# Optimization experiments

Measured on AMD Instinct MI355X. Metric: run time of the kernel, lower is better.

Reference implementation:

```python
import jax, jax.numpy as jnp
import numpy as np

SEQ_LEN = 2048
DIM = 1024
K = 24
N_FFT = 4096  # nearest power of two >= 2*seq_len - 1


def setup_inputs() -> dict:
    key = jax.random.key(0)
    k1, k2, k3, k4 = jax.random.split(key, 4)
    x = jax.random.normal(k1, (4, SEQ_LEN, DIM), dtype=jnp.float32)
    filters = jax.random.normal(k2, (SEQ_LEN, K), dtype=jnp.float32) * 0.1
    M_inputs = jax.random.normal(k3, (DIM, DIM), dtype=jnp.float32) * (DIM ** -0.5)
    M_filters = jax.random.normal(k4, (K, DIM), dtype=jnp.float32) * (K ** -0.5)
    input_pos = jnp.arange(SEQ_LEN, dtype=jnp.int32)
    return {"x": x, "filters": filters, "M_inputs": M_inputs,
            "M_filters": M_filters, "input_pos": input_pos}


def reference(x, filters, M_inputs, M_filters, input_pos):
    # STU forward, use_approx=True, use_hankel_L=False, no flash_fft, no cache.
    B, S, D = x.shape
    # alternating sign +1,-1,+1,... along sequence
    sgn = jnp.where(jnp.arange(S) % 2 == 0, 1.0, -1.0).astype(x.dtype)[None, :, None]
    x_proj = x @ M_inputs                      # (B, S, D)
    phi_proj = filters @ M_filters             # (S, D)
    # v: (1, S, D, 1) -> rfft over seq axis with length N_FFT
    V = jnp.fft.rfft(phi_proj[None, :, :, None], n=N_FFT, axis=1)
    # U: stack [u, u*sgn] on last axis -> (B, S, D, 2)
    U = jnp.fft.rfft(jnp.stack([x_proj, x_proj * sgn], axis=-1), n=N_FFT, axis=1)
    U_conv = jnp.fft.irfft(V * U, n=N_FFT, axis=1)[:, :S]   # (B, S, D, 2)
    spectral_plus = U_conv[..., 0]
    spectral_minus = U_conv[..., 1] * sgn
    return spectral_plus + spectral_minus
```

## Files before the change

kernel.cpp:

```cpp
#include <hip/hip_runtime.h>
#include <hip/hip_bf16.h>
#include <stdint.h>
#include <stddef.h>

#define DIM 1024
#define SEQ 2048
#define KF 24

using f32x4    = __attribute__((ext_vector_type(4))) float;
using bf16x8   = __attribute__((ext_vector_type(8))) short;
using uint32x4 = __attribute__((ext_vector_type(4))) unsigned int;

__device__ __forceinline__ unsigned short f2bf(float f){
  union { float f; unsigned int i; } v; v.f = f;
  unsigned int r = v.i + 0x7FFFu + ((v.i >> 16) & 1u);
  return (unsigned short)(r >> 16);
}
__device__ __forceinline__ float dot2bf(unsigned int a, unsigned int b, float c){
  float d;
  asm("v_dot2_f32_bf16 %0, %1, %2, %3" : "=v"(d) : "v"(a), "v"(b), "v"(c));
  return d;
}
__device__ __forceinline__ unsigned vext(const uint32x4 v, int i){
  return i == 0 ? v.x : i == 1 ? v.y : i == 2 ? v.z : v.w;
}
__device__ __forceinline__ void gload_lds16(const void* g, void* l){
  __builtin_amdgcn_global_load_lds(
      (const __attribute__((address_space(1))) unsigned int*)g,
      (__attribute__((address_space(3))) unsigned int*)l, 16, 0, 0);
}
__device__ __forceinline__ uint32x4 make_srsrc(const void* base, unsigned bytes){
  uint32x4 r;
  r.x = (unsigned)(uintptr_t)base;
  r.y = (unsigned)((uintptr_t)base >> 32);
  r.z = bytes;
  r.w = 0x00020000u;
  return r;
}

__global__ void k_cvt_x(const float* __restrict__ x, unsigned short* __restrict__ xb){
  int i = blockIdx.x * 256 + threadIdx.x;
  const float4* x4 = (const float4*)x;
  float4 v = x4[i];
  ushort4 o;
  o.x = f2bf(v.x); o.y = f2bf(v.y); o.z = f2bf(v.z); o.w = f2bf(v.w);
  *(ushort4*)(xb + (size_t)i * 4) = o;
}

__global__ void k_tr_M(const float* __restrict__ Mi, unsigned short* __restrict__ MbT){
  __shared__ float tile[32][33];
  int e0 = blockIdx.y * 32, d0 = blockIdx.x * 32;
  int tx = threadIdx.x, ty = threadIdx.y;
  #pragma unroll
  for (int r = 0; r < 32; r += 8)
    tile[ty + r][tx] = Mi[(size_t)(e0 + ty + r) * DIM + d0 + tx];
  __syncthreads();
  #pragma unroll
  for (int r = 0; r < 32; r += 8)
    MbT[(size_t)(d0 + ty + r) * DIM + e0 + tx] = f2bf(tile[tx][ty + r]);
}

__global__ void k_pe(const float* __restrict__ filters, const float* __restrict__ Mf,
                     unsigned int* __restrict__ pepkT){
  int r2 = blockIdx.x * 256 + threadIdx.x;
  int d  = blockIdx.y;
  float a0 = 0.f, a1 = 0.f;
  #pragma unroll
  for (int k = 0; k < KF; ++k){
    float mf = Mf[(size_t)k * DIM + d];
    a0 += filters[(size_t)(4 * r2)     * KF + k] * mf;
    a1 += filters[(size_t)(4 * r2 + 2) * KF + k] * mf;
  }
  unsigned int lo = f2bf(2.f * a0), hi = f2bf(2.f * a1);
  pepkT[(size_t)d * 512 + r2] = lo | (hi << 16);
}

#define BM 128
#define BN 128
#define BKK 64
__global__ void k_gemm(const unsigned short* __restrict__ A,
                       const unsigned short* __restrict__ Bt,
                       unsigned int* __restrict__ Bg){
  __shared__ unsigned short As[BM * BKK];
  __shared__ unsigned short Bs[BN * BKK];
  int tid  = threadIdx.x;
  int lane = tid & 63, wave = tid >> 6;
  int wm = wave >> 1, wn = wave & 1;
  int trow0 = blockIdx.x * BM;
  int ncol0 = blockIdx.y * BN;

  f32x4 acc[4][4] = {};

  for (int kt = 0; kt < 1024 / BKK; ++kt){
    __syncthreads();
    #pragma unroll
    for (int g = 0; g < 4; ++g){
      int c  = wave * 4 + g;
      int mr = c * 8 + (lane >> 3);
      int u  = lane & 7;
      int su = u ^ (mr & 7);
      const unsigned short* srcA = A + (size_t)(trow0 + mr) * 1024 + kt * BKK + su * 8;
      gload_lds16(srcA, (char*)As + c * 1024);
      const unsigned short* srcB = Bt + (size_t)(ncol0 + mr) * 1024 + kt * BKK + su * 8;
      gload_lds16(srcB, (char*)Bs + c * 1024);
    }
    __syncthreads();

    bf16x8 af[4][2], bfr[4][2];
    #pragma unroll
    for (int mi = 0; mi < 4; ++mi){
      int row = wm * 64 + mi * 16 + (lane & 15);
      #pragma unroll
      for (int ks = 0; ks < 2; ++ks){
        int u = ((lane >> 4) + 4 * ks) ^ (row & 7);
        af[mi][ks] = *(const bf16x8*)((const char*)As + row * 128 + u * 16);
      }
    }
    #pragma unroll
    for (int ni = 0; ni < 4; ++ni){
      int row = wn * 64 + ni * 16 + (lane & 15);
      #pragma unroll
      for (int ks = 0; ks < 2; ++ks){
        int u = ((lane >> 4) + 4 * ks) ^ (row & 7);
        bfr[ni][ks] = *(const bf16x8*)((const char*)Bs + row * 128 + u * 16);
      }
    }
    #pragma unroll
    for (int mi = 0; mi < 4; ++mi)
      #pragma unroll
      for (int ni = 0; ni < 4; ++ni)
        #pragma unroll
        for (int ks = 0; ks < 2; ++ks)
          acc[mi][ni] = __builtin_amdgcn_mfma_f32_16x16x32_bf16(
              af[mi][ks], bfr[ni][ks], acc[mi][ni], 0, 0, 0);
  }

  unsigned short* Bh = (unsigned short*)Bg;
  #pragma unroll
  for (int mi = 0; mi < 4; ++mi)
    #pragma unroll
    for (int ni = 0; ni < 4; ++ni){
      int col = ncol0 + wn * 64 + ni * 16 + (lane & 15);
      #pragma unroll
      for (int reg = 0; reg < 4; ++reg){
        int row = trow0 + wm * 64 + mi * 16 + (lane >> 4) * 4 + reg;
        unsigned short y = f2bf(acc[mi][ni][reg]);
        int t = row & 2047, bq = row >> 11;
        int p = t & 1, j = t >> 1;
        size_t strm = ((size_t)bq * 2 + p) * 1048576;
        size_t e_lo = strm + (size_t)(j >> 2) * 4096 + (size_t)col * 4 + (j & 3);
        if (j == 0) Bg[e_lo] = (unsigned int)y;
        else        Bh[2 * e_lo] = y;
        if (j < 1023){
          int j1 = j + 1;
          size_t e_hi = strm + (size_t)(j1 >> 2) * 4096 + (size_t)col * 4 + (j1 & 3);
          Bh[2 * e_hi + 1] = y;
        }
      }
    }
}

#define BLX4(dst, so) \
  asm volatile("buffer_load_dwordx4 %0, %1, %2, %3 offen" \
               : "=v"(dst) : "v"(voff), "s"(xrsrc), "s"(so))
#define BLP4_0(dst, so) \
  asm volatile("buffer_load_dwordx4 %0, %1, %2, %3 offen" \
               : "=v"(dst) : "v"(pvoff), "s"(prsrc), "s"(so))
#define BLP4_16(dst, so) \
  asm volatile("buffer_load_dwordx4 %0, %1, %2, %3 offen offset:16" \
               : "=v"(dst) : "v"(pvoff), "s"(prsrc), "s"(so))

__device__ __forceinline__ void phase_old(const uint32x4* BO, const uint32x4* pv,
                                          float* acc){
  #pragma unroll
  for (int q = 0; q < 8; ++q)
    #pragma unroll
    for (int m = 0; m < 32; ++m){
      int idx = m - 2 * q + 16;
      if (idx >= 2 && idx < 16)
        acc[m] = dot2bf(vext(pv[q >> 2], q & 3), vext(BO[(idx >> 2) & 3], idx & 3),
                        acc[m]);
    }
}
__device__ __forceinline__ void phase_mid_new(const uint32x4* BMID, const uint32x4* BNEW,
                                              const uint32x4* pv, float* acc){
  #pragma unroll
  for (int q = 0; q < 8; ++q)
    #pragma unroll
    for (int m = 0; m < 32; ++m){
      int idx = m - 2 * q + 16;
      if (idx >= 16){
        unsigned w = (idx < 32) ? vext(BMID[(idx >> 2) & 3], idx & 3)
                                : vext(BNEW[(idx >> 2) & 3], idx & 3);
        acc[m] = dot2bf(vext(pv[q >> 2], q & 3), w, acc[m]);
      }
    }
}

#define BODY(BO, BMID, BNEW, C) do{                                              \
  phase_old(BO, pv, acc);                                                        \
  __builtin_amdgcn_sched_barrier(0);                                             \
  { unsigned _xs = (unsigned)(4 * (C) + 4) * 16384u;                             \
    BLX4(BO[0], _xs);                                                            \
    BLX4(BO[1], _xs + 16384u);                                                   \
    BLX4(BO[2], _xs + 32768u);                                                   \
    BLX4(BO[3], _xs + 49152u);                                                   \
    unsigned _ps = pbase - 32u * (unsigned)((C) + 1);                            \
    BLP4_0(npv[0], _ps); BLP4_16(npv[1], _ps); }                                 \
  __builtin_amdgcn_sched_barrier(0);                                             \
  phase_mid_new(BMID, BNEW, pv, acc);                                            \
  asm volatile("s_waitcnt vmcnt(0)" ::: "memory");                               \
  __builtin_amdgcn_sched_barrier(0);                                             \
  pv[0] = npv[0]; pv[1] = npv[1];                                                \
}while(0)

__global__ __launch_bounds__(256, 4)
void k_conv(const unsigned int* __restrict__ Bg,
            const unsigned int* __restrict__ pepkT,
            float* __restrict__ out){
  int tid  = threadIdx.x;
  int bid  = blockIdx.x;
  int bp   = bid & 7;
  int rest = bid >> 3;
  int dblk = rest & 3;
  int q    = (rest >> 2) & 7;
  int k4   = rest >> 5;
  int mt   = (k4 == 0) ? q : (k4 == 1) ? 31 - q : (k4 == 2) ? 15 - q : 16 + q;
  int b = bp >> 1, p = bp & 1;
  int d = dblk * 256 + tid;

  uint32x4 xrsrc = make_srsrc(Bg + (size_t)bp * 1048576, 4194304u);
  uint32x4 prsrc = make_srsrc(pepkT, 2097152u);

  unsigned voff  = (unsigned)(d * 16);
  unsigned pvoff = (unsigned)(d * 2048);

  uint32x4 B0[4], B1[4], B2[4], pv[2], npv[2];
  float acc[32];

  unsigned pbase = 64u * (unsigned)mt + 32u;
  int nch = 2 * mt + 2;

  #pragma unroll
  for (int m = 0; m < 32; ++m) acc[m] = 0.f;

  #pragma unroll
  for (int k = 0; k < 4; ++k){
    unsigned s0 = (unsigned)(k - 8) * 16384u;
    BLX4(B0[k], s0);
  }
  #pragma unroll
  for (int k = 0; k < 4; ++k){
    unsigned s1 = (unsigned)(k - 4) * 16384u;
    BLX4(B1[k], s1);
  }
  #pragma unroll
  for (int k = 0; k < 4; ++k){
    unsigned s2 = (unsigned)k * 16384u;
    BLX4(B2[k], s2);
  }
  BLP4_0(pv[0], pbase); BLP4_16(pv[1], pbase);
  asm volatile("s_waitcnt vmcnt(0)" ::: "memory");
  __builtin_amdgcn_sched_barrier(0);

  int c = 0;
  for (;;){
    BODY(B0, B1, B2, c); if (++c == nch) break;
    BODY(B1, B2, B0, c); if (++c == nch) break;
    BODY(B2, B0, B1, c); if (++c == nch) break;
  }

  float* oc = out + ((size_t)(b * SEQ + p) * 1024 + d) + (size_t)mt * 32 * 2048;
  #pragma unroll
  for (int m = 0; m < 32; ++m) oc[(size_t)m * 2048] = acc[m];
}

extern "C" void kernel_launch(void* const* d_in, const int* in_sizes, int n_in,
                              void* d_out, int out_size, void* d_ws, size_t ws_size,
                              hipStream_t stream){
  const float* x       = (const float*)d_in[0];
  const float* filters = (const float*)d_in[1];
  const float* Mi      = (const float*)d_in[2];
  const float* Mf      = (const float*)d_in[3];

  char* ws = (char*)d_ws;
  unsigned short* Xb    = (unsigned short*)(ws);
  unsigned int*   Bg    = (unsigned int*)  (ws + (size_t)16 * 1024 * 1024);
  unsigned short* MbT   = (unsigned short*)(ws + (size_t)48 * 1024 * 1024);
  unsigned int*   pepkT = (unsigned int*)  (ws + (size_t)50 * 1024 * 1024);
  float* out = (float*)d_out;

  hipLaunchKernelGGL(k_cvt_x, dim3(8192), dim3(256), 0, stream, x, Xb);
  hipLaunchKernelGGL(k_tr_M,  dim3(32, 32), dim3(32, 8), 0, stream, Mi, MbT);
  hipLaunchKernelGGL(k_pe,    dim3(2, 1024), dim3(256), 0, stream, filters, Mf, pepkT);
  hipLaunchKernelGGL(k_gemm,  dim3(64, 8), dim3(256), 0, stream, Xb, MbT, Bg);
  hipLaunchKernelGGL(k_conv,  dim3(1024), dim3(256), 0, stream, Bg, pepkT, out);
}
```

Measured before the change: 138.4 us.

## Shrink conv output tile to 16 rows and pair triangular tiles per block

The direct causal convolution kernel now computes 16-row output tiles instead of 32. Each block processes two tiles, s and 63-s, so the triangular work is balanced across blocks. Tile size drops from 32 to 16 accumulators, the X buffers go from three to two, and the filter vectors are double-buffered rather than copied. This cuts register pressure, which may raise occupancy, and evens out per-block work. The cost is more loop-control overhead per unit of work and more reloads of the overlapping X data.

```diff
diff --git a/kernel.cpp b/kernel.cpp
--- a/kernel.cpp
+++ b/kernel.cpp
@@ -170,48 +170,44 @@
   asm volatile("buffer_load_dwordx4 %0, %1, %2, %3 offen offset:16" \
                : "=v"(dst) : "v"(pvoff), "s"(prsrc), "s"(so))
 
-__device__ __forceinline__ void phase_old(const uint32x4* BO, const uint32x4* pv,
-                                          float* acc){
-  #pragma unroll
-  for (int q = 0; q < 8; ++q)
-    #pragma unroll
-    for (int m = 0; m < 32; ++m){
-      int idx = m - 2 * q + 16;
-      if (idx >= 2 && idx < 16)
-        acc[m] = dot2bf(vext(pv[q >> 2], q & 3), vext(BO[(idx >> 2) & 3], idx & 3),
-                        acc[m]);
-    }
-}
-__device__ __forceinline__ void phase_mid_new(const uint32x4* BMID, const uint32x4* BNEW,
-                                              const uint32x4* pv, float* acc){
-  #pragma unroll
-  for (int q = 0; q < 8; ++q)
-    #pragma unroll
-    for (int m = 0; m < 32; ++m){
-      int idx = m - 2 * q + 16;
-      if (idx >= 16){
-        unsigned w = (idx < 32) ? vext(BMID[(idx >> 2) & 3], idx & 3)
-                                : vext(BNEW[(idx >> 2) & 3], idx & 3);
-        acc[m] = dot2bf(vext(pv[q >> 2], q & 3), w, acc[m]);
-      }
-    }
-}
-
-#define BODY(BO, BMID, BNEW, C) do{                                              \
-  phase_old(BO, pv, acc);                                                        \
+__device__ __forceinline__ void phase_new16(const uint32x4* XBN, const uint32x4* PV,
+                                            float* acc){
+  #pragma unroll
+  for (int qq = 0; qq < 8; ++qq)
+    #pragma unroll
+    for (int m = 0; m < 16; ++m){
+      int idx = m - 2 * qq + 16;
+      if (idx >= 16)
+        acc[m] = dot2bf(vext(PV[qq >> 2], qq & 3),
+                        vext(XBN[(idx - 16) >> 2], idx & 3), acc[m]);
+    }
+}
+__device__ __forceinline__ void phase_old16(const uint32x4* XBO, const uint32x4* PV,
+                                            float* acc){
+  #pragma unroll
+  for (int qq = 0; qq < 8; ++qq)
+    #pragma unroll
+    for (int m = 0; m < 16; ++m){
+      int idx = m - 2 * qq + 16;
+      if (idx < 16)
+        acc[m] = dot2bf(vext(PV[qq >> 2], qq & 3),
+                        vext(XBO[idx >> 2], idx & 3), acc[m]);
+    }
+}
+
+#define CH(XBN_, XBO_, PVA, PVB, XS, PS) do{                                     \
+  phase_new16(XBN_, PVA, acc);                                                   \
   __builtin_amdgcn_sched_barrier(0);                                             \
-  { unsigned _xs = (unsigned)(4 * (C) + 4) * 16384u;                             \
-    BLX4(BO[0], _xs);                                                            \
-    BLX4(BO[1], _xs + 16384u);                                                   \
-    BLX4(BO[2], _xs + 32768u);                                                   \
-    BLX4(BO[3], _xs + 49152u);                                                   \
-    unsigned _ps = pbase - 32u * (unsigned)((C) + 1);                            \
-    BLP4_0(npv[0], _ps); BLP4_16(npv[1], _ps); }                                 \
+  BLX4(XBN_[0], (XS));                                                           \
+  BLX4(XBN_[1], (XS) + 16384u);                                                  \
+  BLX4(XBN_[2], (XS) + 32768u);                                                  \
+  BLX4(XBN_[3], (XS) + 49152u);                                                  \
+  BLP4_0 (PVB[0], (PS));                                                         \
+  BLP4_16(PVB[1], (PS));                                                         \
   __builtin_amdgcn_sched_barrier(0);                                             \
-  phase_mid_new(BMID, BNEW, pv, acc);                                            \
+  phase_old16(XBO_, PVA, acc);                                                   \
   asm volatile("s_waitcnt vmcnt(0)" ::: "memory");                               \
   __builtin_amdgcn_sched_barrier(0);                                             \
-  pv[0] = npv[0]; pv[1] = npv[1];                                                \
 }while(0)
 
 __global__ __launch_bounds__(256, 4)
@@ -223,9 +219,7 @@
   int bp   = bid & 7;
   int rest = bid >> 3;
   int dblk = rest & 3;
-  int q    = (rest >> 2) & 7;
-  int k4   = rest >> 5;
-  int mt   = (k4 == 0) ? q : (k4 == 1) ? 31 - q : (k4 == 2) ? 15 - q : 16 + q;
+  int sp   = rest >> 2;
   int b = bp >> 1, p = bp & 1;
   int d = dblk * 256 + tid;
 
@@ -235,44 +229,38 @@
   unsigned voff  = (unsigned)(d * 16);
   unsigned pvoff = (unsigned)(d * 2048);
 
-  uint32x4 B0[4], B1[4], B2[4], pv[2], npv[2];
-  float acc[32];
-
-  unsigned pbase = 64u * (unsigned)mt + 32u;
-  int nch = 2 * mt + 2;
-
-  #pragma unroll
-  for (int m = 0; m < 32; ++m) acc[m] = 0.f;
-
-  #pragma unroll
-  for (int k = 0; k < 4; ++k){
-    unsigned s0 = (unsigned)(k - 8) * 16384u;
-    BLX4(B0[k], s0);
+  uint32x4 X0[4], X1[4], pva[2], pvb[2];
+  float acc[16];
+  float* outb = out + ((size_t)(b * SEQ + p) * 1024 + d);
+
+  #pragma unroll
+  for (int ti = 0; ti < 2; ++ti){
+    int s = ti ? (63 - sp) : sp;
+
+    #pragma unroll
+    for (int m = 0; m < 16; ++m) acc[m] = 0.f;
+
+    #pragma unroll
+    for (int k = 0; k < 4; ++k) BLX4(X0[k], (unsigned)(4 * s + k) * 16384u);
+    #pragma unroll
+    for (int k = 0; k < 4; ++k) BLX4(X1[k], (unsigned)(4 * s - 4 + k) * 16384u);
+    BLP4_0(pva[0], 0u); BLP4_16(pva[1], 0u);
+    asm volatile("s_waitcnt vmcnt(0)" ::: "memory");
+    __builtin_amdgcn_sched_barrier(0);
+
+    unsigned ps = 32u;
+    int u = s;
+    for (;;){
+      unsigned xs = (unsigned)(4 * u - 8) * 16384u;
+      CH(X0, X1, pva, pvb, xs, ps); ps += 32u; if (--u < 0) break;
+      xs = (unsigned)(4 * u - 8) * 16384u;
+      CH(X1, X0, pvb, pva, xs, ps); ps += 32u; if (--u < 0) break;
+    }
+
+    float* oc = outb + (size_t)s * 16 * 2048;
+    #pragma unroll
+    for (int m = 0; m < 16; ++m) oc[(size_t)m * 2048] = acc[m];
   }
-  #pragma unroll
-  for (int k = 0; k < 4; ++k){
-    unsigned s1 = (unsigned)(k - 4) * 16384u;
-    BLX4(B1[k], s1);
-  }
-  #pragma unroll
-  for (int k = 0; k < 4; ++k){
-    unsigned s2 = (unsigned)k * 16384u;
-    BLX4(B2[k], s2);
-  }
-  BLP4_0(pv[0], pbase); BLP4_16(pv[1], pbase);
-  asm volatile("s_waitcnt vmcnt(0)" ::: "memory");
-  __builtin_amdgcn_sched_barrier(0);
-
-  int c = 0;
-  for (;;){
-    BODY(B0, B1, B2, c); if (++c == nch) break;
-    BODY(B1, B2, B0, c); if (++c == nch) break;
-    BODY(B2, B0, B1, c); if (++c == nch) break;
-  }
-
-  float* oc = out + ((size_t)(b * SEQ + p) * 1024 + d) + (size_t)mt * 32 * 2048;
-  #pragma unroll
-  for (int m = 0; m < 32; ++m) oc[(size_t)m * 2048] = acc[m];
 }
 
 extern "C" void kernel_launch(void* const* d_in, const int* in_sizes, int n_in,
```

Result: slower. 176.4 us (+27.4%).
